# Kernel optimization log

Measured on AMD Instinct MI355X. Metric: run time of the kernel, lower is better.

## Reference

```python
import jax, jax.numpy as jnp
import numpy as np

T, B, N, C, H = 4, 32, 256, 384, 8
D = C // H
TAU = 2.0
EPS = 1e-5
SCALE = C ** -0.5

# --- surrogate-gradient spike (spikingjelly Sigmoid surrogate, alpha=4) ---
@jax.custom_vjp
def spike(x):
    return (x >= 0.0).astype(x.dtype)

def _spike_fwd(x):
    return spike(x), x

def _spike_bwd(x, g):
    s = jax.nn.sigmoid(4.0 * x)
    return (g * 4.0 * s * (1.0 - s),)

spike.defvjp(_spike_fwd, _spike_bwd)

def lif(x):
    # MultiStepLIFNode: v' = v + (x - (v - v_reset))/tau, v_reset=0, v_th=1, hard reset, detach_reset
    def step(v, xt):
        h = v + (xt - v) / TAU
        s = spike(h - 1.0)
        v_next = h * (1.0 - jax.lax.stop_gradient(s))
        return v_next, s
    _, spikes = jax.lax.scan(step, jnp.zeros_like(x[0]), x)
    return spikes

def bn_c(x, gamma, beta, mean, var):
    # BatchNorm1d over channel dim C in eval mode; x: [TB, N, C]
    return (x - mean) * (gamma * jax.lax.rsqrt(var + EPS)) + beta

def setup_inputs() -> dict:
    key = jax.random.key(0)
    ks = jax.random.split(key, 10)
    x = jax.random.normal(ks[0], (T, B, N, C), jnp.float32)
    def w(k):
        return jax.random.normal(k, (C, C), jnp.float32) * (C ** -0.5)
    def bn(k):
        kg, kb, km, kv = jax.random.split(k, 4)
        return jnp.stack([
            1.0 + 0.1 * jax.random.normal(kg, (C,), jnp.float32),
            0.1 * jax.random.normal(kb, (C,), jnp.float32),
            0.1 * jax.random.normal(km, (C,), jnp.float32),
            jax.random.uniform(kv, (C,), jnp.float32, 0.5, 1.5),
        ])  # [gamma, beta, running_mean, running_var]
    rel_table = 0.02 * jax.random.normal(ks[9], (2 * N - 1, H), jnp.float32)
    return {
        "x": x,
        "w_q": w(ks[1]), "w_k": w(ks[2]), "w_v": w(ks[3]), "w_p": w(ks[4]),
        "bn_q": bn(ks[5]), "bn_k": bn(ks[6]), "bn_v": bn(ks[7]), "bn_p": bn(ks[8]),
        "rel_table": rel_table,
    }

def reference(x, w_q, w_k, w_v, w_p, bn_q, bn_k, bn_v, bn_p, rel_table):
    xf = x.reshape(T * B, N, C)

    def branch(w, bnp):
        y = bn_c(xf @ w.T, *bnp).reshape(T, B, N, C)
        y = lif(y)
        return y.reshape(T, B, N, H, D).transpose(0, 1, 3, 2, 4)  # [T,B,H,N,D]

    q = branch(w_q, bn_q)
    k = branch(w_k, bn_k)
    v = branch(w_v, bn_v)

    scores = jnp.einsum('tbhnd,tbhmd->tbhnm', q, k)  # [T,B,H,N,N]
    # relative bias: idx[i,j] = i - j + N - 1
    idx = jnp.arange(N)[:, None] - jnp.arange(N)[None, :] + N - 1
    bias = rel_table[idx]  # [N,N,H]
    scores = scores + bias.transpose(2, 0, 1)[None, None]

    out = jnp.einsum('tbhnm,tbhmd->tbhnd', scores, v) * SCALE
    out = out.transpose(0, 1, 3, 2, 4).reshape(T, B, N, C)
    out = lif(out)  # attn_lif

    y = bn_c(out.reshape(T * B, N, C) @ w_p.T, *bn_p).reshape(T, B, N, C)
    return lif(y)  # proj_lif; dropout is eval-mode identity
```

## Files before the change

### kernel.cpp

```cpp
#include <hip/hip_runtime.h>
#include <stdint.h>

#define T_ 4
#define B_ 32
#define N_ 256
#define C_ 384
#define H_ 8
#define D_ 48
#define ROWS (B_*N_)
#define SCALE_F 0.051031036307982884f

#define QS_OFF 0u
#define KS_OFF 25165824u
#define VS_OFF 50331648u
#define AS_OFF 75497472u
#define WH_OFF 0u
#define WM_OFF 294912u
#define WL_OFF 589824u

typedef __bf16 bf16x8 __attribute__((ext_vector_type(8)));
typedef float  f32x4  __attribute__((ext_vector_type(4)));

__device__ __forceinline__ void split3(float s, uint32_t& h, uint32_t& m, uint32_t& l) {
    uint32_t u  = __float_as_uint(s);
    uint32_t hu = u & 0xffff0000u;
    float r1 = s - __uint_as_float(hu);
    uint32_t u1 = __float_as_uint(r1);
    uint32_t mu = u1 & 0xffff0000u;
    float r2 = r1 - __uint_as_float(mu);
    h = hu >> 16; m = mu >> 16; l = __float_as_uint(r2) >> 16;
}

__global__ void k_wsplit3(const float* __restrict__ wq, const float* __restrict__ wk,
                          const float* __restrict__ wv, uint16_t* __restrict__ out)
{
    const int br = blockIdx.y;
    const float* __restrict__ w = (br==0)? wq : (br==1)? wk : wv;
    const int idx = blockIdx.x*256 + threadIdx.x;
    uint32_t h, m, l;
    split3(w[idx], h, m, l);
    uint16_t* base = out + (size_t)br*442368;
    base[idx] = (uint16_t)h;
    base[147456 + idx] = (uint16_t)m;
    base[294912 + idx] = (uint16_t)l;
}

__global__ __launch_bounds__(256, 3) void k_qkv_mfma(
    const float* __restrict__ x, const uint16_t* __restrict__ wbr,
    const float* __restrict__ bnq, const float* __restrict__ bnk, const float* __restrict__ bnv,
    uint16_t* __restrict__ qs, uint16_t* __restrict__ ks, uint16_t* __restrict__ vs)
{
    const int cb = blockIdx.x;
    const int branch = cb / 3;
    const int ct = cb - branch*3;
    const int c0 = ct * 128;
    const int bn0 = blockIdx.y * 32;
    const float* __restrict__ bnp_ = (branch==0)? bnq : (branch==1)? bnk : bnv;
    uint16_t* __restrict__ outp = (branch==0)? qs : (branch==1)? ks : vs;
    const uint16_t* __restrict__ wpl = wbr + (size_t)branch*442368;

    __shared__ __align__(16) uint16_t At[128][104];
    __shared__ __align__(16) uint16_t Bt[128][104];

    const int tid  = threadIdx.x;
    const int wv   = tid >> 6;
    const int lane = tid & 63;
    const int l15  = lane & 15;
    const int quad = lane >> 4;
    const int q8   = quad * 8;
    const int rg   = wv >> 1;
    const int wcol = (wv & 1) * 64;

    f32x4 acc[4][4];
    #pragma unroll
    for (int it=0; it<4; ++it)
        #pragma unroll
        for (int jt=0; jt<4; ++jt) acc[it][jt] = (f32x4){0.f,0.f,0.f,0.f};

    const int trow = tid >> 1, half = tid & 1;
    const int tA = trow >> 5, bnlA = trow & 31;
    const float* xrow = x + ((size_t)(tA*ROWS + bn0 + bnlA))*C_ + half*16;

    for (int kt=0; kt<12; ++kt) {
        const int k0 = kt*32;
        __syncthreads();
        {
            float4 f0 = *(const float4*)(xrow + k0);
            float4 f1 = *(const float4*)(xrow + k0 + 4);
            float4 f2 = *(const float4*)(xrow + k0 + 8);
            float4 f3 = *(const float4*)(xrow + k0 + 12);
            float fe[16];
            *(float4*)&fe[0] = f0; *(float4*)&fe[4] = f1;
            *(float4*)&fe[8] = f2; *(float4*)&fe[12] = f3;
            uint32_t hw[8], mw[8], lw[8];
            #pragma unroll
            for (int i=0; i<8; ++i) {
                const float s0 = fe[2*i], s1 = fe[2*i+1];
                const uint32_t h0 = __float_as_uint(s0) & 0xffff0000u;
                const uint32_t h1 = __float_as_uint(s1) & 0xffff0000u;
                const float r0 = s0 - __uint_as_float(h0);
                const float r1 = s1 - __uint_as_float(h1);
                const uint32_t m0 = __float_as_uint(r0) & 0xffff0000u;
                const uint32_t m1 = __float_as_uint(r1) & 0xffff0000u;
                const float p0 = r0 - __uint_as_float(m0);
                const float p1 = r1 - __uint_as_float(m1);
                hw[i] = (h0>>16) | h1;
                mw[i] = (m0>>16) | m1;
                lw[i] = (__float_as_uint(p0)>>16) | (__float_as_uint(p1) & 0xffff0000u);
            }
            *(uint4*)&At[trow][ 0 + half*16]     = make_uint4(hw[0],hw[1],hw[2],hw[3]);
            *(uint4*)&At[trow][ 0 + half*16 + 8] = make_uint4(hw[4],hw[5],hw[6],hw[7]);
            *(uint4*)&At[trow][32 + half*16]     = make_uint4(mw[0],mw[1],mw[2],mw[3]);
            *(uint4*)&At[trow][32 + half*16 + 8] = make_uint4(mw[4],mw[5],mw[6],mw[7]);
            *(uint4*)&At[trow][64 + half*16]     = make_uint4(lw[0],lw[1],lw[2],lw[3]);
            *(uint4*)&At[trow][64 + half*16 + 8] = make_uint4(lw[4],lw[5],lw[6],lw[7]);
        }
        #pragma unroll
        for (int rep=0; rep<6; ++rep) {
            const int id = rep*256 + tid;
            const int p = id >> 9, rem = id & 511, c = rem >> 2, ks8 = rem & 3;
            *(uint4*)&Bt[c][p*32 + ks8*8] =
                *(const uint4*)(wpl + (size_t)p*147456 + (size_t)(c0 + c)*C_ + k0 + ks8*8);
        }
        __syncthreads();

        bf16x8 af[4][3];
        #pragma unroll
        for (int it=0; it<4; ++it) {
            const uint16_t* ar = &At[rg*64 + it*16 + l15][q8];
            af[it][0] = *(const bf16x8*)(ar);
            af[it][1] = *(const bf16x8*)(ar + 32);
            af[it][2] = *(const bf16x8*)(ar + 64);
        }
        #pragma unroll
        for (int jt=0; jt<4; ++jt) {
            const uint16_t* bb = &Bt[wcol + jt*16 + l15][q8];
            const bf16x8 b0 = *(const bf16x8*)(bb);
            const bf16x8 b1 = *(const bf16x8*)(bb + 32);
            const bf16x8 b2 = *(const bf16x8*)(bb + 64);
            #pragma unroll
            for (int it=0; it<4; ++it) {
                f32x4 a = acc[it][jt];
                a = __builtin_amdgcn_mfma_f32_16x16x32_bf16(af[it][0], b0, a, 0,0,0);
                a = __builtin_amdgcn_mfma_f32_16x16x32_bf16(af[it][0], b1, a, 0,0,0);
                a = __builtin_amdgcn_mfma_f32_16x16x32_bf16(af[it][1], b0, a, 0,0,0);
                a = __builtin_amdgcn_mfma_f32_16x16x32_bf16(af[it][0], b2, a, 0,0,0);
                a = __builtin_amdgcn_mfma_f32_16x16x32_bf16(af[it][1], b1, a, 0,0,0);
                a = __builtin_amdgcn_mfma_f32_16x16x32_bf16(af[it][2], b0, a, 0,0,0);
                acc[it][jt] = a;
            }
        }
    }

    __syncthreads();
    float* vex = (float*)&At[0][0];

    #define STORE_SP(tt, sp) do { \
        if (branch == 2) { \
            const int h2 = cg / 48, dd = cg - h2*48; \
            const int bng = bn0 + bnl; \
            outp[((((size_t)(tt)*B_ + (bng>>8))*H_ + h2)*D_ + dd)*N_ + (bng&255)] = (sp); \
        } else { \
            outp[((size_t)((tt)*ROWS + bn0 + bnl))*C_ + cg] = (sp); \
        } \
    } while(0)

    if (rg == 0) {
        #pragma unroll
        for (int jt=0; jt<4; ++jt) {
            const int cl = wcol + jt*16 + l15;
            const int cg = c0 + cl;
            const float g = bnp_[cg], be = bnp_[C_+cg], mu = bnp_[2*C_+cg], va = bnp_[3*C_+cg];
            const float scl = g * (float)(1.0 / sqrt((double)(va + 1e-5f)));
            #pragma unroll
            for (int a=0; a<2; ++a)
                #pragma unroll
                for (int r=0; r<4; ++r) {
                    const int bnl = a*16 + quad*4 + r;
                    const float y0 = (acc[a  ][jt][r] - mu)*scl + be;
                    const float y1 = (acc[a+2][jt][r] - mu)*scl + be;
                    float v = 0.f;
                    float h = v + (y0 - v)*0.5f;
                    STORE_SP(0, (h >= 1.0f) ? (uint16_t)0x3f80 : (uint16_t)0);
                    v = (h >= 1.0f) ? 0.f : h;
                    h = v + (y1 - v)*0.5f;
                    STORE_SP(1, (h >= 1.0f) ? (uint16_t)0x3f80 : (uint16_t)0);
                    v = (h >= 1.0f) ? 0.f : h;
                    vex[bnl*128 + cl] = v;
                }
        }
    }
    __syncthreads();
    if (rg == 1) {
        #pragma unroll
        for (int jt=0; jt<4; ++jt) {
            const int cl = wcol + jt*16 + l15;
            const int cg = c0 + cl;
            const float g = bnp_[cg], be = bnp_[C_+cg], mu = bnp_[2*C_+cg], va = bnp_[3*C_+cg];
            const float scl = g * (float)(1.0 / sqrt((double)(va + 1e-5f)));
            #pragma unroll
            for (int a=0; a<2; ++a)
                #pragma unroll
                for (int r=0; r<4; ++r) {
                    const int bnl = a*16 + quad*4 + r;
                    const float y2 = (acc[a  ][jt][r] - mu)*scl + be;
                    const float y3 = (acc[a+2][jt][r] - mu)*scl + be;
                    float v = vex[bnl*128 + cl];
                    float h = v + (y2 - v)*0.5f;
                    STORE_SP(2, (h >= 1.0f) ? (uint16_t)0x3f80 : (uint16_t)0);
                    v = (h >= 1.0f) ? 0.f : h;
                    h = v + (y3 - v)*0.5f;
                    STORE_SP(3, (h >= 1.0f) ? (uint16_t)0x3f80 : (uint16_t)0);
                }
        }
    }
    #undef STORE_SP
}

__global__ __launch_bounds__(256, 2) void k_attn(
    const uint16_t* __restrict__ qs, const uint16_t* __restrict__ ks, const uint16_t* __restrict__ vs,
    const float* __restrict__ rel, uint16_t* __restrict__ as_)
{
    const int bh = blockIdx.x;
    const int b = bh >> 3, h = bh & 7;
    const int i0 = blockIdx.y * 128;

    __shared__ __align__(16) uint16_t qt[128][72];
    __shared__ __align__(16) uint16_t kt[32][72];
    __shared__ __align__(16) uint16_t vT[48][40];
    __shared__ __align__(16) uint16_t sh[3][128][40];
    __shared__ float tab_s[384];

    const int tid  = threadIdx.x;
    const int wv_  = tid >> 6;
    const int lane = tid & 63;
    const int l15  = lane & 15;
    const int quad = lane >> 4;
    const int w32  = wv_ * 32;
    const int q8   = quad * 8;

    for (int l = tid; l < 383; l += 256) tab_s[l] = rel[(size_t)(i0 + l)*H_ + h];
    {
        const uint4 z = make_uint4(0,0,0,0);
        { const int row = tid >> 1, seg = tid & 1;
          *(uint4*)&qt[row][48 + seg*8] = z; }
        if (tid < 64) { const int row = tid >> 1, seg = tid & 1;
          *(uint4*)&kt[row][48 + seg*8] = z; }
    }

    float vst[2][3][4];
    #pragma unroll
    for (int a=0;a<2;++a)
        #pragma unroll
        for (int e=0;e<3;++e)
            #pragma unroll
            for (int r=0;r<4;++r) vst[a][e][r]=0.f;

    for (int t=0; t<4; ++t) {
        const int tb = t*B_ + b;
        __syncthreads();
        #pragma unroll
        for (int rep=0; rep<3; ++rep) {
            const int l = rep*256 + tid;
            const int row = l / 6, seg = l - 6*row;
            *(uint4*)&qt[row][seg*8] =
                *(const uint4*)(qs + ((size_t)(tb*N_ + i0 + row))*C_ + h*D_ + seg*8);
        }

        f32x4 pacc[2][3];
        #pragma unroll
        for (int a=0;a<2;++a)
            #pragma unroll
            for (int e=0;e<3;++e) pacc[a][e] = (f32x4){0.f,0.f,0.f,0.f};

        for (int j0 = 0; j0 < 256; j0 += 32) {
            __syncthreads();
            if (tid < 192) {
                const int row = tid / 6, seg = tid - 6*row;
                *(uint4*)&kt[row][seg*8] =
                    *(const uint4*)(ks + ((size_t)(tb*N_ + j0 + row))*C_ + h*D_ + seg*8);
            } else {
                const int l = tid - 192;
                #pragma unroll
                for (int rep=0; rep<3; ++rep) {
                    const int e = rep*64 + l;
                    const int d = e >> 2, seg = e & 3;
                    *(uint4*)&vT[d][seg*8] =
                        *(const uint4*)(vs + (((size_t)(tb*H_ + h))*D_ + d)*N_ + j0 + seg*8);
                }
            }
            __syncthreads();

            f32x4 sacc[2][2];
            #pragma unroll
            for (int a=0;a<2;++a)
                #pragma unroll
                for (int c2=0;c2<2;++c2) sacc[a][c2] = (f32x4){0.f,0.f,0.f,0.f};
            bf16x8 qa[2][2];
            #pragma unroll
            for (int it=0; it<2; ++it)
                #pragma unroll
                for (int ks_=0; ks_<2; ++ks_)
                    qa[it][ks_] = *(const bf16x8*)&qt[w32 + it*16 + l15][ks_*32 + q8];
            #pragma unroll
            for (int jt=0; jt<2; ++jt) {
                #pragma unroll
                for (int ks_=0; ks_<2; ++ks_) {
                    const bf16x8 kb = *(const bf16x8*)&kt[jt*16 + l15][ks_*32 + q8];
                    #pragma unroll
                    for (int it=0; it<2; ++it)
                        sacc[it][jt] = __builtin_amdgcn_mfma_f32_16x16x32_bf16(
                            qa[it][ks_], kb, sacc[it][jt], 0, 0, 0);
                }
            }

            #pragma unroll
            for (int it=0; it<2; ++it)
                #pragma unroll
                for (int jt=0; jt<2; ++jt) {
                    const int jl = jt*16 + l15;
                    const int jg = j0 + jl;
                    #pragma unroll
                    for (int r=0; r<4; ++r) {
                        const int il = w32 + it*16 + quad*4 + r;
                        const float s = sacc[it][jt][r] + tab_s[il - jg + 255];
                        uint32_t hh, mm, ll;
                        split3(s, hh, mm, ll);
                        sh[0][il][jl] = (uint16_t)hh;
                        sh[1][il][jl] = (uint16_t)mm;
                        sh[2][il][jl] = (uint16_t)ll;
                    }
                }

            bf16x8 vb[3];
            #pragma unroll
            for (int dt=0; dt<3; ++dt)
                vb[dt] = *(const bf16x8*)&vT[dt*16 + l15][q8];
            #pragma unroll
            for (int it=0; it<2; ++it)
                #pragma unroll
                for (int p=0; p<3; ++p) {
                    const bf16x8 sa = *(const bf16x8*)&sh[p][w32 + it*16 + l15][q8];
                    #pragma unroll
                    for (int dt=0; dt<3; ++dt)
                        pacc[it][dt] = __builtin_amdgcn_mfma_f32_16x16x32_bf16(
                            sa, vb[dt], pacc[it][dt], 0, 0, 0);
                }
        }

        #pragma unroll
        for (int it=0; it<2; ++it)
            #pragma unroll
            for (int dt=0; dt<3; ++dt)
                #pragma unroll
                for (int r=0; r<4; ++r) {
                    const float xin = pacc[it][dt][r] * SCALE_F;
                    float v = vst[it][dt][r];
                    const float hh = v + (xin - v)*0.5f;
                    const uint16_t sp = (hh >= 1.0f) ? (uint16_t)0x3f80 : (uint16_t)0;
                    vst[it][dt][r] = (hh >= 1.0f) ? 0.f : hh;
                    const int ig = i0 + w32 + it*16 + quad*4 + r;
                    const int c  = h*D_ + dt*16 + l15;
                    as_[((size_t)(tb*N_ + ig))*C_ + c] = sp;
                }
    }
}

__global__ void k_wsplit(const float* __restrict__ wp,
                         uint16_t* __restrict__ wh, uint16_t* __restrict__ wm,
                         uint16_t* __restrict__ wl)
{
    const int idx = blockIdx.x*256 + threadIdx.x;
    uint32_t h, m, l;
    split3(wp[idx], h, m, l);
    wh[idx] = (uint16_t)h; wm[idx] = (uint16_t)m; wl[idx] = (uint16_t)l;
}

__global__ __launch_bounds__(256, 2) void k_proj(
    const uint16_t* __restrict__ as_,
    const uint16_t* __restrict__ wh, const uint16_t* __restrict__ wm,
    const uint16_t* __restrict__ wl,
    const float* __restrict__ bnp, float* __restrict__ out)
{
    const int r0 = blockIdx.x * 64;
    const int c0 = blockIdx.y * 96;

    __shared__ __align__(16) uint16_t At[4][64][40];
    __shared__ __align__(16) uint16_t Bt[3][96][40];

    const int tid  = threadIdx.x;
    const int wv_  = tid >> 6;
    const int lane = tid & 63;
    const int l15  = lane & 15;
    const int quad = lane >> 4;
    const int q8   = quad * 8;

    f32x4 acc[4][6];
    #pragma unroll
    for (int t=0;t<4;++t)
        #pragma unroll
        for (int nt=0;nt<6;++nt) acc[t][nt] = (f32x4){0.f,0.f,0.f,0.f};

    for (int kstep=0; kstep<12; ++kstep) {
        const int k0 = kstep*32;
        __syncthreads();
        #pragma unroll
        for (int rep=0; rep<4; ++rep) {
            const int l = rep*256 + tid;
            const int t = l >> 8, row = (l >> 2) & 63, seg = l & 3;
            *(uint4*)&At[t][row][seg*8] =
                *(const uint4*)(as_ + ((size_t)(t*ROWS + r0 + row))*C_ + k0 + seg*8);
        }
        for (int l = tid; l < 1152; l += 256) {
            const int p = l / 384, rem = l - 384*p;
            const int c = rem >> 2, seg = rem & 3;
            const uint16_t* src = (p==0)? wh : (p==1)? wm : wl;
            *(uint4*)&Bt[p][c][seg*8] =
                *(const uint4*)(src + (size_t)(c0 + c)*C_ + k0 + seg*8);
        }
        __syncthreads();

        bf16x8 af[4];
        #pragma unroll
        for (int t=0;t<4;++t)
            af[t] = *(const bf16x8*)&At[t][wv_*16 + l15][q8];
        #pragma unroll
        for (int nt=0; nt<6; ++nt) {
            #pragma unroll
            for (int p=0; p<3; ++p) {
                const bf16x8 bf_ = *(const bf16x8*)&Bt[p][nt*16 + l15][q8];
                #pragma unroll
                for (int t=0;t<4;++t)
                    acc[t][nt] = __builtin_amdgcn_mfma_f32_16x16x32_bf16(
                        af[t], bf_, acc[t][nt], 0, 0, 0);
            }
        }
    }

    #pragma unroll
    for (int nt=0; nt<6; ++nt) {
        const int c = c0 + nt*16 + l15;
        const float g = bnp[c], be = bnp[C_+c], mu = bnp[2*C_+c], va = bnp[3*C_+c];
        const float scl = g * (float)(1.0 / sqrt((double)(va + 1e-5f)));
        #pragma unroll
        for (int r=0; r<4; ++r) {
            const int rg = r0 + wv_*16 + quad*4 + r;
            float v = 0.f;
            #pragma unroll
            for (int t=0; t<4; ++t) {
                const float y  = (acc[t][nt][r] - mu)*scl + be;
                const float hh = v + (y - v)*0.5f;
                const float sp = (hh >= 1.0f) ? 1.0f : 0.f;
                v = (hh >= 1.0f) ? 0.f : hh;
                out[((size_t)(t*ROWS + rg))*C_ + c] = sp;
            }
        }
    }
}

extern "C" void kernel_launch(void* const* d_in, const int* in_sizes, int n_in,
                              void* d_out, int out_size, void* d_ws, size_t ws_size,
                              hipStream_t stream) {
    const float* x   = (const float*)d_in[0];
    const float* wq  = (const float*)d_in[1];
    const float* wk  = (const float*)d_in[2];
    const float* wv  = (const float*)d_in[3];
    const float* wp  = (const float*)d_in[4];
    const float* bnq = (const float*)d_in[5];
    const float* bnk = (const float*)d_in[6];
    const float* bnv = (const float*)d_in[7];
    const float* bnp = (const float*)d_in[8];
    const float* rel = (const float*)d_in[9];
    float* out = (float*)d_out;
    uint8_t* ws = (uint8_t*)d_ws;
    uint16_t* qs  = (uint16_t*)(ws + QS_OFF);
    uint16_t* ks  = (uint16_t*)(ws + KS_OFF);
    uint16_t* vs  = (uint16_t*)(ws + VS_OFF);
    uint16_t* as_ = (uint16_t*)(ws + AS_OFF);
    uint16_t* wbr = (uint16_t*)(ws + AS_OFF);
    uint16_t* wh  = (uint16_t*)(ws + WH_OFF);
    uint16_t* wm  = (uint16_t*)(ws + WM_OFF);
    uint16_t* wl  = (uint16_t*)(ws + WL_OFF);

    k_wsplit3 <<<dim3(576, 3), 256, 0, stream>>>(wq, wk, wv, wbr);
    k_qkv_mfma<<<dim3(9, 256), 256, 0, stream>>>(x, wbr, bnq, bnk, bnv, qs, ks, vs);
    k_attn    <<<dim3(256, 2), 256, 0, stream>>>(qs, ks, vs, rel, as_);
    k_wsplit  <<<dim3(576),    256, 0, stream>>>(wp, wh, wm, wl);
    k_proj    <<<dim3(128, 4), 256, 0, stream>>>(as_, wh, wm, wl, bnp, out);
}
```

Before: 402.5 us.

## Double the row tile of QKV projection GEMM to 256 rows per block

Adds a QKV projection kernel that processes 64 (b,n) positions times 4 timesteps (256 rows) per block instead of 32, so each weight tile loaded into LDS is reused across twice as many rows. It halves the grid, doubles accumulators per wave, and needs dynamic LDS (about 78KB), enabled through a one-time function attribute with a fallback to the old kernel. The LIF epilogue is split between two wave groups, handing the membrane state across timesteps through LDS. The cost is higher register pressure and lower occupancy (launch bound 2).

After: 399.0 us. About the same (-0.9%).

```diff
diff --git a/kernel.cpp b/kernel.cpp
--- a/kernel.cpp
+++ b/kernel.cpp
@@ -43,6 +43,177 @@
     base[idx] = (uint16_t)h;
     base[147456 + idx] = (uint16_t)m;
     base[294912 + idx] = (uint16_t)l;
+}
+
+#define SA 104
+
+__global__ __launch_bounds__(256, 2) void k_qkv_mfma256(
+    const float* __restrict__ x, const uint16_t* __restrict__ wbr,
+    const float* __restrict__ bnq, const float* __restrict__ bnk, const float* __restrict__ bnv,
+    uint16_t* __restrict__ qs, uint16_t* __restrict__ ks, uint16_t* __restrict__ vs)
+{
+    extern __shared__ uint16_t smem[];
+    uint16_t (*At)[SA] = (uint16_t (*)[SA])smem;
+    uint16_t (*Bt)[SA] = (uint16_t (*)[SA])(smem + 256*SA);
+
+    const int cb = blockIdx.x;
+    const int branch = cb / 3;
+    const int ct = cb - branch*3;
+    const int c0 = ct * 128;
+    const int bn0 = blockIdx.y * 64;
+    const float* __restrict__ bnp_ = (branch==0)? bnq : (branch==1)? bnk : bnv;
+    uint16_t* __restrict__ outp = (branch==0)? qs : (branch==1)? ks : vs;
+    const uint16_t* __restrict__ wpl = wbr + (size_t)branch*442368;
+
+    const int tid  = threadIdx.x;
+    const int wv   = tid >> 6;
+    const int lane = tid & 63;
+    const int l15  = lane & 15;
+    const int quad = lane >> 4;
+    const int q8   = quad * 8;
+    const int rg   = wv >> 1;
+    const int wcol = (wv & 1) * 64;
+
+    f32x4 acc[8][4];
+    #pragma unroll
+    for (int it=0; it<8; ++it)
+        #pragma unroll
+        for (int jt=0; jt<4; ++jt) acc[it][jt] = (f32x4){0.f,0.f,0.f,0.f};
+
+    const int tA = tid >> 6, bnlA = tid & 63;
+    const float* xrow = x + ((size_t)(tA*ROWS + bn0 + bnlA))*C_;
+
+    for (int kt=0; kt<12; ++kt) {
+        const int k0 = kt*32;
+        __syncthreads();
+        {
+            float fe[32];
+            #pragma unroll
+            for (int s=0; s<8; ++s)
+                *(float4*)&fe[4*s] = *(const float4*)(xrow + k0 + 4*s);
+            uint32_t hw[16], mw[16], lw[16];
+            #pragma unroll
+            for (int i=0; i<16; ++i) {
+                const float s0 = fe[2*i], s1 = fe[2*i+1];
+                const uint32_t h0 = __float_as_uint(s0) & 0xffff0000u;
+                const uint32_t h1 = __float_as_uint(s1) & 0xffff0000u;
+                const float r0 = s0 - __uint_as_float(h0);
+                const float r1 = s1 - __uint_as_float(h1);
+                const uint32_t m0 = __float_as_uint(r0) & 0xffff0000u;
+                const uint32_t m1 = __float_as_uint(r1) & 0xffff0000u;
+                const float p0 = r0 - __uint_as_float(m0);
+                const float p1 = r1 - __uint_as_float(m1);
+                hw[i] = (h0>>16) | h1;
+                mw[i] = (m0>>16) | m1;
+                lw[i] = (__float_as_uint(p0)>>16) | (__float_as_uint(p1) & 0xffff0000u);
+            }
+            #pragma unroll
+            for (int s=0; s<4; ++s) {
+                *(uint4*)&At[tid][     s*8] = make_uint4(hw[4*s],hw[4*s+1],hw[4*s+2],hw[4*s+3]);
+                *(uint4*)&At[tid][32 + s*8] = make_uint4(mw[4*s],mw[4*s+1],mw[4*s+2],mw[4*s+3]);
+                *(uint4*)&At[tid][64 + s*8] = make_uint4(lw[4*s],lw[4*s+1],lw[4*s+2],lw[4*s+3]);
+            }
+        }
+        #pragma unroll
+        for (int rep=0; rep<6; ++rep) {
+            const int id = rep*256 + tid;
+            const int p = id >> 9, rem = id & 511, c = rem >> 2, ks8 = rem & 3;
+            *(uint4*)&Bt[c][p*32 + ks8*8] =
+                *(const uint4*)(wpl + (size_t)p*147456 + (size_t)(c0 + c)*C_ + k0 + ks8*8);
+        }
+        __syncthreads();
+
+        bf16x8 bfr[4][3];
+        #pragma unroll
+        for (int jt=0; jt<4; ++jt) {
+            const uint16_t* bb = &Bt[wcol + jt*16 + l15][q8];
+            bfr[jt][0] = *(const bf16x8*)(bb);
+            bfr[jt][1] = *(const bf16x8*)(bb + 32);
+            bfr[jt][2] = *(const bf16x8*)(bb + 64);
+        }
+        #pragma unroll
+        for (int it=0; it<8; ++it) {
+            const uint16_t* ar = &At[rg*128 + it*16 + l15][q8];
+            const bf16x8 a0 = *(const bf16x8*)(ar);
+            const bf16x8 a1 = *(const bf16x8*)(ar + 32);
+            const bf16x8 a2 = *(const bf16x8*)(ar + 64);
+            #pragma unroll
+            for (int jt=0; jt<4; ++jt) {
+                f32x4 a = acc[it][jt];
+                a = __builtin_amdgcn_mfma_f32_16x16x32_bf16(a0, bfr[jt][0], a, 0,0,0);
+                a = __builtin_amdgcn_mfma_f32_16x16x32_bf16(a0, bfr[jt][1], a, 0,0,0);
+                a = __builtin_amdgcn_mfma_f32_16x16x32_bf16(a1, bfr[jt][0], a, 0,0,0);
+                a = __builtin_amdgcn_mfma_f32_16x16x32_bf16(a0, bfr[jt][2], a, 0,0,0);
+                a = __builtin_amdgcn_mfma_f32_16x16x32_bf16(a1, bfr[jt][1], a, 0,0,0);
+                a = __builtin_amdgcn_mfma_f32_16x16x32_bf16(a2, bfr[jt][0], a, 0,0,0);
+                acc[it][jt] = a;
+            }
+        }
+    }
+
+    __syncthreads();
+    float* vex = (float*)smem;
+
+    #define STORE_SP(tt, sp) do { \
+        if (branch == 2) { \
+            const int h2 = cg / 48, dd = cg - h2*48; \
+            const int bng = bn0 + bnl; \
+            outp[((((size_t)(tt)*B_ + (bng>>8))*H_ + h2)*D_ + dd)*N_ + (bng&255)] = (sp); \
+        } else { \
+            outp[((size_t)((tt)*ROWS + bn0 + bnl))*C_ + cg] = (sp); \
+        } \
+    } while(0)
+
+    if (rg == 0) {
+        #pragma unroll
+        for (int jt=0; jt<4; ++jt) {
+            const int cl = wcol + jt*16 + l15;
+            const int cg = c0 + cl;
+            const float g = bnp_[cg], be = bnp_[C_+cg], mu = bnp_[2*C_+cg], va = bnp_[3*C_+cg];
+            const float scl = g * (float)(1.0 / sqrt((double)(va + 1e-5f)));
+            #pragma unroll
+            for (int a=0; a<4; ++a)
+                #pragma unroll
+                for (int r=0; r<4; ++r) {
+                    const int bnl = a*16 + quad*4 + r;
+                    const float y0 = (acc[a  ][jt][r] - mu)*scl + be;
+                    const float y1 = (acc[4+a][jt][r] - mu)*scl + be;
+                    float v = 0.f;
+                    float h = v + (y0 - v)*0.5f;
+                    STORE_SP(0, (h >= 1.0f) ? (uint16_t)0x3f80 : (uint16_t)0);
+                    v = (h >= 1.0f) ? 0.f : h;
+                    h = v + (y1 - v)*0.5f;
+                    STORE_SP(1, (h >= 1.0f) ? (uint16_t)0x3f80 : (uint16_t)0);
+                    v = (h >= 1.0f) ? 0.f : h;
+                    vex[bnl*128 + cl] = v;
+                }
+        }
+    }
+    __syncthreads();
+    if (rg == 1) {
+        #pragma unroll
+        for (int jt=0; jt<4; ++jt) {
+            const int cl = wcol + jt*16 + l15;
+            const int cg = c0 + cl;
+            const float g = bnp_[cg], be = bnp_[C_+cg], mu = bnp_[2*C_+cg], va = bnp_[3*C_+cg];
+            const float scl = g * (float)(1.0 / sqrt((double)(va + 1e-5f)));
+            #pragma unroll
+            for (int a=0; a<4; ++a)
+                #pragma unroll
+                for (int r=0; r<4; ++r) {
+                    const int bnl = a*16 + quad*4 + r;
+                    const float y2 = (acc[a  ][jt][r] - mu)*scl + be;
+                    const float y3 = (acc[4+a][jt][r] - mu)*scl + be;
+                    float v = vex[bnl*128 + cl];
+                    float h = v + (y2 - v)*0.5f;
+                    STORE_SP(2, (h >= 1.0f) ? (uint16_t)0x3f80 : (uint16_t)0);
+                    v = (h >= 1.0f) ? 0.f : h;
+                    h = v + (y3 - v)*0.5f;
+                    STORE_SP(3, (h >= 1.0f) ? (uint16_t)0x3f80 : (uint16_t)0);
+                }
+        }
+    }
+    #undef STORE_SP
 }
 
 __global__ __launch_bounds__(256, 3) void k_qkv_mfma(
@@ -85,13 +256,10 @@
         const int k0 = kt*32;
         __syncthreads();
         {
-            float4 f0 = *(const float4*)(xrow + k0);
-            float4 f1 = *(const float4*)(xrow + k0 + 4);
-            float4 f2 = *(const float4*)(xrow + k0 + 8);
-            float4 f3 = *(const float4*)(xrow + k0 + 12);
             float fe[16];
-            *(float4*)&fe[0] = f0; *(float4*)&fe[4] = f1;
-            *(float4*)&fe[8] = f2; *(float4*)&fe[12] = f3;
+            #pragma unroll
+            for (int s=0; s<4; ++s)
+                *(float4*)&fe[4*s] = *(const float4*)(xrow + k0 + 4*s);
             uint32_t hw[8], mw[8], lw[8];
             #pragma unroll
             for (int i=0; i<8; ++i) {
@@ -457,6 +625,17 @@
         }
     }
 }
+
+#define QKV256_LDS_BYTES ((256 + 128) * SA * 2)
+struct BigLdsInit {
+    bool ok;
+    BigLdsInit() {
+        ok = (hipFuncSetAttribute((const void*)k_qkv_mfma256,
+                                  hipFuncAttributeMaxDynamicSharedMemorySize,
+                                  QKV256_LDS_BYTES) == hipSuccess);
+    }
+};
+static BigLdsInit g_biglds;
 
 extern "C" void kernel_launch(void* const* d_in, const int* in_sizes, int n_in,
                               void* d_out, int out_size, void* d_ws, size_t ws_size,
@@ -483,7 +662,12 @@
     uint16_t* wl  = (uint16_t*)(ws + WL_OFF);
 
     k_wsplit3 <<<dim3(576, 3), 256, 0, stream>>>(wq, wk, wv, wbr);
-    k_qkv_mfma<<<dim3(9, 256), 256, 0, stream>>>(x, wbr, bnq, bnk, bnv, qs, ks, vs);
+    if (g_biglds.ok) {
+        k_qkv_mfma256<<<dim3(9, 128), 256, QKV256_LDS_BYTES, stream>>>(
+            x, wbr, bnq, bnk, bnv, qs, ks, vs);
+    } else {
+        k_qkv_mfma<<<dim3(9, 256), 256, 0, stream>>>(x, wbr, bnq, bnk, bnv, qs, ks, vs);
+    }
     k_attn    <<<dim3(256, 2), 256, 0, stream>>>(qs, ks, vs, rel, as_);
     k_wsplit  <<<dim3(576),    256, 0, stream>>>(wp, wh, wm, wl);
     k_proj    <<<dim3(128, 4), 256, 0, stream>>>(as_, wh, wm, wl, bnp, out);
```

## Load QKV weight fragments directly from global memory and prefetch next x tile

Applied to the files above, without the earlier changes.

The QKV projection kernel no longer stages the split bf16 weight planes through a shared-memory tile. Each lane instead loads its MFMA B fragments straight from global memory (L2-resident weights). The x row chunk for the next k-step is also prefetched into registers before the MFMAs of the current step, to overlap global latency. This halves LDS use, which may allow more occupancy and removes LDS write/read traffic, but each wave now issues its own uncoalesced-ish global loads and loses reuse of the weight tile across the waves of the block.

Result: slower. 435.3 us (+8.2%).

```diff
diff --git a/kernel.cpp b/kernel.cpp
--- a/kernel.cpp
+++ b/kernel.cpp
@@ -45,7 +45,9 @@
     base[294912 + idx] = (uint16_t)l;
 }
 
-__global__ __launch_bounds__(256, 3) void k_qkv_mfma(
+#define SA 104
+
+__global__ __launch_bounds__(256, 3) void k_qkv_v5(
     const float* __restrict__ x, const uint16_t* __restrict__ wbr,
     const float* __restrict__ bnq, const float* __restrict__ bnk, const float* __restrict__ bnv,
     uint16_t* __restrict__ qs, uint16_t* __restrict__ ks, uint16_t* __restrict__ vs)
@@ -59,8 +61,7 @@
     uint16_t* __restrict__ outp = (branch==0)? qs : (branch==1)? ks : vs;
     const uint16_t* __restrict__ wpl = wbr + (size_t)branch*442368;
 
-    __shared__ __align__(16) uint16_t At[128][104];
-    __shared__ __align__(16) uint16_t Bt[128][104];
+    __shared__ __align__(16) uint16_t At[128][SA];
 
     const int tid  = threadIdx.x;
     const int wv   = tid >> 6;
@@ -81,17 +82,20 @@
     const int tA = trow >> 5, bnlA = trow & 31;
     const float* xrow = x + ((size_t)(tA*ROWS + bn0 + bnlA))*C_ + half*16;
 
+    const uint16_t* bbase[4];
+    #pragma unroll
+    for (int jt=0; jt<4; ++jt)
+        bbase[jt] = wpl + (size_t)(c0 + wcol + jt*16 + l15)*C_ + q8;
+
+    float fe[16];
+    #pragma unroll
+    for (int s=0; s<4; ++s)
+        *(float4*)&fe[4*s] = *(const float4*)(xrow + 4*s);
+
     for (int kt=0; kt<12; ++kt) {
         const int k0 = kt*32;
         __syncthreads();
         {
-            float4 f0 = *(const float4*)(xrow + k0);
-            float4 f1 = *(const float4*)(xrow + k0 + 4);
-            float4 f2 = *(const float4*)(xrow + k0 + 8);
-            float4 f3 = *(const float4*)(xrow + k0 + 12);
-            float fe[16];
-            *(float4*)&fe[0] = f0; *(float4*)&fe[4] = f1;
-            *(float4*)&fe[8] = f2; *(float4*)&fe[12] = f3;
             uint32_t hw[8], mw[8], lw[8];
             #pragma unroll
             for (int i=0; i<8; ++i) {
@@ -115,15 +119,22 @@
             *(uint4*)&At[trow][64 + half*16]     = make_uint4(lw[0],lw[1],lw[2],lw[3]);
             *(uint4*)&At[trow][64 + half*16 + 8] = make_uint4(lw[4],lw[5],lw[6],lw[7]);
         }
-        #pragma unroll
-        for (int rep=0; rep<6; ++rep) {
-            const int id = rep*256 + tid;
-            const int p = id >> 9, rem = id & 511, c = rem >> 2, ks8 = rem & 3;
-            *(uint4*)&Bt[c][p*32 + ks8*8] =
-                *(const uint4*)(wpl + (size_t)p*147456 + (size_t)(c0 + c)*C_ + k0 + ks8*8);
-        }
         __syncthreads();
 
+        if (kt < 11) {
+            const float* xn = xrow + (kt+1)*32;
+            #pragma unroll
+            for (int s=0; s<4; ++s)
+                *(float4*)&fe[4*s] = *(const float4*)(xn + 4*s);
+        }
+
+        bf16x8 bfr[4][3];
+        #pragma unroll
+        for (int jt=0; jt<4; ++jt) {
+            bfr[jt][0] = *(const bf16x8*)(bbase[jt] + k0);
+            bfr[jt][1] = *(const bf16x8*)(bbase[jt] + 147456 + k0);
+            bfr[jt][2] = *(const bf16x8*)(bbase[jt] + 294912 + k0);
+        }
         bf16x8 af[4][3];
         #pragma unroll
         for (int it=0; it<4; ++it) {
@@ -134,19 +145,15 @@
         }
         #pragma unroll
         for (int jt=0; jt<4; ++jt) {
-            const uint16_t* bb = &Bt[wcol + jt*16 + l15][q8];
-            const bf16x8 b0 = *(const bf16x8*)(bb);
-            const bf16x8 b1 = *(const bf16x8*)(bb + 32);
-            const bf16x8 b2 = *(const bf16x8*)(bb + 64);
             #pragma unroll
             for (int it=0; it<4; ++it) {
                 f32x4 a = acc[it][jt];
-                a = __builtin_amdgcn_mfma_f32_16x16x32_bf16(af[it][0], b0, a, 0,0,0);
-                a = __builtin_amdgcn_mfma_f32_16x16x32_bf16(af[it][0], b1, a, 0,0,0);
-                a = __builtin_amdgcn_mfma_f32_16x16x32_bf16(af[it][1], b0, a, 0,0,0);
-                a = __builtin_amdgcn_mfma_f32_16x16x32_bf16(af[it][0], b2, a, 0,0,0);
-                a = __builtin_amdgcn_mfma_f32_16x16x32_bf16(af[it][1], b1, a, 0,0,0);
-                a = __builtin_amdgcn_mfma_f32_16x16x32_bf16(af[it][2], b0, a, 0,0,0);
+                a = __builtin_amdgcn_mfma_f32_16x16x32_bf16(af[it][0], bfr[jt][0], a, 0,0,0);
+                a = __builtin_amdgcn_mfma_f32_16x16x32_bf16(af[it][0], bfr[jt][1], a, 0,0,0);
+                a = __builtin_amdgcn_mfma_f32_16x16x32_bf16(af[it][1], bfr[jt][0], a, 0,0,0);
+                a = __builtin_amdgcn_mfma_f32_16x16x32_bf16(af[it][0], bfr[jt][2], a, 0,0,0);
+                a = __builtin_amdgcn_mfma_f32_16x16x32_bf16(af[it][1], bfr[jt][1], a, 0,0,0);
+                a = __builtin_amdgcn_mfma_f32_16x16x32_bf16(af[it][2], bfr[jt][0], a, 0,0,0);
                 acc[it][jt] = a;
             }
         }
@@ -482,9 +489,9 @@
     uint16_t* wm  = (uint16_t*)(ws + WM_OFF);
     uint16_t* wl  = (uint16_t*)(ws + WL_OFF);
 
-    k_wsplit3 <<<dim3(576, 3), 256, 0, stream>>>(wq, wk, wv, wbr);
-    k_qkv_mfma<<<dim3(9, 256), 256, 0, stream>>>(x, wbr, bnq, bnk, bnv, qs, ks, vs);
-    k_attn    <<<dim3(256, 2), 256, 0, stream>>>(qs, ks, vs, rel, as_);
-    k_wsplit  <<<dim3(576),    256, 0, stream>>>(wp, wh, wm, wl);
-    k_proj    <<<dim3(128, 4), 256, 0, stream>>>(as_, wh, wm, wl, bnp, out);
-}
+    k_wsplit3<<<dim3(576, 3), 256, 0, stream>>>(wq, wk, wv, wbr);
+    k_qkv_v5 <<<dim3(9, 256), 256, 0, stream>>>(x, wbr, bnq, bnk, bnv, qs, ks, vs);
+    k_attn   <<<dim3(256, 2), 256, 0, stream>>>(qs, ks, vs, rel, as_);
+    k_wsplit <<<dim3(576),    256, 0, stream>>>(wp, wh, wm, wl);
+    k_proj   <<<dim3(128, 4), 256, 0, stream>>>(as_, wh, wm, wl, bnp, out);
+}
```
